# Optimization experiments

Measured on AMD Instinct MI355X. Metric: run time of the kernel, lower is better.

## Reference

```python
import jax, jax.numpy as jnp
import numpy as np

B, T, P, V, D, DINO, H, L = 32, 40, 256, 4096, 256, 384, 4, 2
HD = D // H          # head dim 64
DFF = 4 * D          # 1024
EPS = 1e-5


def setup_inputs() -> dict:
    key = jax.random.key(0)
    ks = iter(jax.random.split(key, 40))
    rn = lambda shape, s=0.02: jax.random.normal(next(ks), shape, jnp.float32) * s
    return dict(
        patches=jax.random.normal(next(ks), (B, P, DINO), jnp.float32),
        tokens=jax.random.randint(next(ks), (B, T), 0, V, jnp.int32),
        tok_emb=rn((V, D)),
        pos_emb=rn((1, T, D)),
        qkv_w=rn((L, 3 * D, D)), qkv_b=jnp.zeros((L, 3 * D), jnp.float32),
        out_w=rn((L, D, D)), out_b=jnp.zeros((L, D), jnp.float32),
        ln1_s=jnp.ones((L, D), jnp.float32), ln1_b=jnp.zeros((L, D), jnp.float32),
        w1=rn((L, DFF, D)), b1=jnp.zeros((L, DFF), jnp.float32),
        w2=rn((L, D, DFF)), b2=jnp.zeros((L, D), jnp.float32),
        ln2_s=jnp.ones((L, D), jnp.float32), ln2_b=jnp.zeros((L, D), jnp.float32),
        fus_w1=rn((D, DINO + D)), fus_b1=jnp.zeros((D,), jnp.float32),
        fus_w2=rn((D, D)), fus_b2=jnp.zeros((D,), jnp.float32),
        cls_w=rn((V, D)), cls_b=jnp.zeros((V,), jnp.float32),
    )


def _ln(x, s, b):
    m = jnp.mean(x, -1, keepdims=True)
    v = jnp.var(x, -1, keepdims=True)
    return (x - m) * jax.lax.rsqrt(v + EPS) * s + b


def _token_encoder(tokens, tok_emb, pos_emb, qkv_w, qkv_b, out_w, out_b,
                   ln1_s, ln1_b, w1, b1, w2, b2, ln2_s, ln2_b):
    # Causal full-sequence pass: output at position t equals re-running the
    # unmasked encoder on tokens[:, :t+1] and taking the last position.
    x = tok_emb[tokens] + pos_emb[:, :tokens.shape[1], :]   # [B,T,D]
    causal = jnp.triu(jnp.full((T, T), -1e9, jnp.float32), 1)  # [T,T]
    for l in range(L):  # fixed small layer count
        qkv = x @ qkv_w[l].T + qkv_b[l]                     # [B,T,3D]
        q, k, v = jnp.split(qkv, 3, axis=-1)
        q = q.reshape(B, T, H, HD).transpose(0, 2, 1, 3)    # [B,H,T,hd]
        k = k.reshape(B, T, H, HD).transpose(0, 2, 1, 3)
        v = v.reshape(B, T, H, HD).transpose(0, 2, 1, 3)
        scores = jnp.einsum('bhqd,bhkd->bhqk', q, k) / np.sqrt(HD).astype(np.float32)
        attn = jax.nn.softmax(scores + causal, axis=-1)
        ctx = jnp.einsum('bhqk,bhkd->bhqd', attn, v)        # [B,H,T,hd]
        ctx = ctx.transpose(0, 2, 1, 3).reshape(B, T, D)
        x = _ln(x + ctx @ out_w[l].T + out_b[l], ln1_s[l], ln1_b[l])
        h = jax.nn.relu(x @ w1[l].T + b1[l]) @ w2[l].T + b2[l]
        x = _ln(x + h, ln2_s[l], ln2_b[l])
    return x  # [B,T,D]


def reference(patches, tokens, tok_emb, pos_emb, qkv_w, qkv_b, out_w, out_b,
              ln1_s, ln1_b, w1, b1, w2, b2, ln2_s, ln2_b,
              fus_w1, fus_b1, fus_w2, fus_b2, cls_w, cls_b):
    enc = _token_encoder(tokens, tok_emb, pos_emb, qkv_w, qkv_b, out_w, out_b,
                         ln1_s, ln1_b, w1, b1, w2, b2, ln2_s, ln2_b)  # [B,T,D]
    # context for step 0 is zeros; step t>0 uses encoder output at position t-1
    ctx = jnp.concatenate([jnp.zeros((B, 1, D), enc.dtype), enc[:, :-1]], axis=1)  # [B,T,D]
    # fusion MLP: split the concat-linear into a patch part and a context part
    wp, wc = fus_w1[:, :DINO], fus_w1[:, DINO:]
    pproj = patches @ wp.T                                  # [B,P,D]
    cproj = ctx @ wc.T + fus_b1                             # [B,T,D]
    h = jax.nn.gelu(pproj[:, None, :, :] + cproj[:, :, None, :], approximate=False)  # [B,T,P,D]
    fused = h @ fus_w2.T + fus_b2                           # [B,T,P,D]
    # sigmoid+gather of the 4096-way logits == gather classifier rows, dot, sigmoid
    w_sel = cls_w[tokens]                                   # [B,T,D]
    b_sel = cls_b[tokens]                                   # [B,T]
    logits = jnp.einsum('btpd,btd->btp', fused, w_sel) + b_sel[:, :, None]
    probs = jax.nn.sigmoid(logits)                          # [B,T,P]
    return probs.transpose(0, 2, 1)                         # [B,P,T] == [B,256,40]
```

## Files before the change

### kernel.cpp

```cpp
#include <hip/hip_runtime.h>
#include <hip/hip_bf16.h>

#define B_ 32
#define T_ 40
#define P_ 256
#define V_ 4096
#define D_ 256
#define DINO_ 384
#define H_ 4
#define L_ 2
#define HD_ 64
#define DFF_ 1024
#define EPS_ 1e-5f

typedef __bf16 bf16;
typedef __bf16 bf16x8 __attribute__((ext_vector_type(8)));
typedef float f32x4 __attribute__((ext_vector_type(4)));

#define OFF_QKV 0
#define OFF_OUTW 393216
#define OFF_W1 524288
#define OFF_W2 1048576
#define OFF_FUS 1572864
#define WB_TOTAL 1736704
#define CONV_BLOCKS 848
#define PAT_BLOCKS 1536

__device__ __forceinline__ bf16x8 cvt8(const float* p) {
  float4 f0 = *(const float4*)p;
  float4 f1 = *(const float4*)(p + 4);
  bf16x8 v;
  v[0] = (bf16)f0.x; v[1] = (bf16)f0.y; v[2] = (bf16)f0.z; v[3] = (bf16)f0.w;
  v[4] = (bf16)f1.x; v[5] = (bf16)f1.y; v[6] = (bf16)f1.z; v[7] = (bf16)f1.w;
  return v;
}

__global__ __launch_bounds__(256) void prep_k(
    const int* __restrict__ tokens, const float* __restrict__ tok_emb,
    const float* __restrict__ pos_emb, float* __restrict__ x,
    const float* __restrict__ fus_w2, bf16* __restrict__ w2Tb,
    const float* __restrict__ qkv_w, const float* __restrict__ out_w,
    const float* __restrict__ w1, const float* __restrict__ w2,
    const float* __restrict__ fus_w1, bf16* __restrict__ wb,
    const float* __restrict__ patches, bf16* __restrict__ patb) {
  __shared__ float tile[32][33];
  int bi = blockIdx.x;
  int tid = threadIdx.x;
  if (bi < B_ * T_) {
    int t = bi % T_;
    x[bi * D_ + tid] = tok_emb[tokens[bi] * D_ + tid] + pos_emb[t * D_ + tid];
  } else if (bi < B_ * T_ + 64) {
    int tt = bi - B_ * T_;
    int bx = (tt & 7) * 32, by = (tt >> 3) * 32;
    int tx = tid & 31, ty = tid >> 5;
#pragma unroll
    for (int i = 0; i < 32; i += 8) tile[ty + i][tx] = fus_w2[(by + ty + i) * D_ + bx + tx];
    __syncthreads();
#pragma unroll
    for (int i = 0; i < 32; i += 8)
      w2Tb[(bx + ty + i) * D_ + by + tx] = (bf16)tile[tx][ty + i];
  } else if (bi < B_ * T_ + 64 + CONV_BLOCKS) {
    long f = (long)(bi - B_ * T_ - 64) * 2048 + tid * 8;
    const float* src;
    long off;
    if (f < OFF_OUTW)      { src = qkv_w;  off = f - OFF_QKV; }
    else if (f < OFF_W1)   { src = out_w;  off = f - OFF_OUTW; }
    else if (f < OFF_W2)   { src = w1;     off = f - OFF_W1; }
    else if (f < OFF_FUS)  { src = w2;     off = f - OFF_W2; }
    else                   { src = fus_w1; off = f - OFF_FUS; }
    *(bf16x8*)&wb[f] = cvt8(src + off);
  } else {
    long f = (long)(bi - B_ * T_ - 64 - CONV_BLOCKS) * 2048 + tid * 8;
    *(bf16x8*)&patb[f] = cvt8(patches + f);
  }
}

template <int ABF16, int OBF16, int RELU>
__global__ __launch_bounds__(256) void gemm64_k(
    const void* __restrict__ Av, const bf16* __restrict__ W,
    const float* __restrict__ bias, void* __restrict__ outv,
    int K, int lda, int ldw, int ldc) {
  __shared__ bf16 As[64 * 72];
  __shared__ bf16 Ws[64 * 72];
  const int tid = threadIdx.x;
  const int lane = tid & 63;
  const int wv = tid >> 6;
  const int col = lane & 15, quad = lane >> 4;
  const int bn = blockIdx.x * 64, bm = blockIdx.y * 64;
  const float* Af = (const float*)Av;
  const bf16* Ab = (const bf16*)Av;

  f32x4 acc[4];
#pragma unroll
  for (int i = 0; i < 4; ++i) acc[i] = (f32x4){0.f, 0.f, 0.f, 0.f};

  for (int kk = 0; kk < K; kk += 64) {
#pragma unroll
    for (int it = 0; it < 2; ++it) {
      int c = tid + it * 256;
      int row = c >> 3, kc = (c & 7) * 8;
      if (ABF16)
        *(bf16x8*)&As[row * 72 + kc] = *(const bf16x8*)(Ab + (long)(bm + row) * lda + kk + kc);
      else
        *(bf16x8*)&As[row * 72 + kc] = cvt8(Af + (long)(bm + row) * lda + kk + kc);
      *(bf16x8*)&Ws[row * 72 + kc] = *(const bf16x8*)(W + (long)(bn + row) * ldw + kk + kc);
    }
    __syncthreads();
#pragma unroll
    for (int ki = 0; ki < 2; ++ki) {
      bf16x8 bfr = *(const bf16x8*)&Ws[(wv * 16 + col) * 72 + ki * 32 + quad * 8];
#pragma unroll
      for (int i = 0; i < 4; ++i) {
        bf16x8 afr = *(const bf16x8*)&As[(i * 16 + col) * 72 + ki * 32 + quad * 8];
        acc[i] = __builtin_amdgcn_mfma_f32_16x16x32_bf16(afr, bfr, acc[i], 0, 0, 0);
      }
    }
    __syncthreads();
  }
  const int n = bn + wv * 16 + col;
  float bv = bias ? bias[n] : 0.0f;
#pragma unroll
  for (int i = 0; i < 4; ++i) {
#pragma unroll
    for (int r = 0; r < 4; ++r) {
      int m = bm + i * 16 + quad * 4 + r;
      float val = acc[i][r] + bv;
      if (RELU) val = fmaxf(val, 0.0f);
      if (OBF16) ((bf16*)outv)[(long)m * ldc + n] = (bf16)val;
      else ((float*)outv)[(long)m * ldc + n] = val;
    }
  }
}

template <int ABF16>
__global__ __launch_bounds__(256) void gemmln_k(
    const void* __restrict__ Av, const bf16* __restrict__ W,
    const float* __restrict__ bias, const float* __restrict__ resid,
    const float* __restrict__ lng, const float* __restrict__ lnb,
    float* __restrict__ xout, int K) {
  __shared__ bf16 As[32 * 72];
  __shared__ bf16 Ws[256 * 72];
  __shared__ float2 wred[4][32];
  const int tid = threadIdx.x;
  const int lane = tid & 63;
  const int wv = tid >> 6;
  const int col = lane & 15, quad = lane >> 4;
  const int bm = blockIdx.x * 32;
  const int srow = tid >> 3, kc = (tid & 7) * 8;
  const float* Af = (const float*)Av;
  const bf16* Ab = (const bf16*)Av;

  f32x4 acc[2][4];
#pragma unroll
  for (int mt = 0; mt < 2; ++mt)
#pragma unroll
    for (int nt = 0; nt < 4; ++nt) acc[mt][nt] = (f32x4){0.f, 0.f, 0.f, 0.f};

  for (int kk = 0; kk < K; kk += 64) {
    if (ABF16)
      *(bf16x8*)&As[srow * 72 + kc] = *(const bf16x8*)(Ab + (long)(bm + srow) * K + kk + kc);
    else
      *(bf16x8*)&As[srow * 72 + kc] = cvt8(Af + (long)(bm + srow) * K + kk + kc);
#pragma unroll
    for (int i = 0; i < 8; ++i) {
      int c = tid + i * 256;
      int r = c >> 3, k2 = (c & 7) * 8;
      *(bf16x8*)&Ws[r * 72 + k2] = *(const bf16x8*)(W + (long)r * K + kk + k2);
    }
    __syncthreads();
#pragma unroll
    for (int ki = 0; ki < 2; ++ki) {
#pragma unroll
      for (int nt = 0; nt < 4; ++nt) {
        bf16x8 bfr = *(const bf16x8*)&Ws[(wv * 64 + nt * 16 + col) * 72 + ki * 32 + quad * 8];
#pragma unroll
        for (int mt = 0; mt < 2; ++mt) {
          bf16x8 afr = *(const bf16x8*)&As[(mt * 16 + col) * 72 + ki * 32 + quad * 8];
          acc[mt][nt] = __builtin_amdgcn_mfma_f32_16x16x32_bf16(afr, bfr, acc[mt][nt], 0, 0, 0);
        }
      }
    }
    __syncthreads();
  }

  float biasv[4], gv[4], bvv[4];
#pragma unroll
  for (int nt = 0; nt < 4; ++nt) {
    int n = wv * 64 + nt * 16 + col;
    biasv[nt] = bias[n];
    gv[nt] = lng[n];
    bvv[nt] = lnb[n];
  }
  float rsum[2][4], rss[2][4];
#pragma unroll
  for (int mt = 0; mt < 2; ++mt)
#pragma unroll
    for (int r = 0; r < 4; ++r) {
      int m = bm + mt * 16 + quad * 4 + r;
      float s = 0.f, q = 0.f;
#pragma unroll
      for (int nt = 0; nt < 4; ++nt) {
        int n = wv * 64 + nt * 16 + col;
        float v = acc[mt][nt][r] + biasv[nt] + resid[(long)m * D_ + n];
        acc[mt][nt][r] = v;
        s += v;
        q += v * v;
      }
      rsum[mt][r] = s;
      rss[mt][r] = q;
    }
#pragma unroll
  for (int mk = 1; mk < 16; mk <<= 1)
#pragma unroll
    for (int mt = 0; mt < 2; ++mt)
#pragma unroll
      for (int r = 0; r < 4; ++r) {
        rsum[mt][r] += __shfl_xor(rsum[mt][r], mk);
        rss[mt][r] += __shfl_xor(rss[mt][r], mk);
      }
  if (col == 0) {
#pragma unroll
    for (int mt = 0; mt < 2; ++mt)
#pragma unroll
      for (int r = 0; r < 4; ++r) {
        float2 p; p.x = rsum[mt][r]; p.y = rss[mt][r];
        wred[wv][mt * 16 + quad * 4 + r] = p;
      }
  }
  __syncthreads();
#pragma unroll
  for (int mt = 0; mt < 2; ++mt)
#pragma unroll
    for (int r = 0; r < 4; ++r) {
      int ml = mt * 16 + quad * 4 + r;
      float s = 0.f, q = 0.f;
#pragma unroll
      for (int w = 0; w < 4; ++w) {
        float2 p = wred[w][ml];
        s += p.x;
        q += p.y;
      }
      float mean = s * (1.0f / D_);
      float inv = rsqrtf(q * (1.0f / D_) - mean * mean + EPS_);
#pragma unroll
      for (int nt = 0; nt < 4; ++nt) {
        int n = wv * 64 + nt * 16 + col;
        xout[(long)(bm + ml) * D_ + n] =
            (acc[mt][nt][r] - mean) * inv * gv[nt] + bvv[nt];
      }
    }
}

__global__ __launch_bounds__(256) void attn_k(const float* __restrict__ qkv,
                                              float* __restrict__ ctx) {
  __shared__ float q[20][HD_ + 1];
  __shared__ float k[T_][HD_ + 1];
  __shared__ float v[T_][HD_ + 1];
  __shared__ float s[20][T_ + 1];
  int h = blockIdx.x, b = blockIdx.y, zq = blockIdx.z;
  int r0 = zq * 20;
  int tid = threadIdx.x;
  for (int idx = tid; idx < T_ * HD_; idx += 256) {
    int t = idx >> 6, d = idx & 63;
    long base = (long)(b * T_ + t) * (3 * D_) + h * HD_ + d;
    k[t][d] = qkv[base + D_];
    v[t][d] = qkv[base + 2 * D_];
    if (t < 20) q[t][d] = qkv[(long)(b * T_ + r0 + t) * (3 * D_) + h * HD_ + d];
  }
  __syncthreads();
  for (int idx = tid; idx < 20 * T_; idx += 256) {
    int i = idx / T_, j = idx - i * T_;
    if (j <= r0 + i) {
      float acc = 0.f;
#pragma unroll
      for (int d = 0; d < HD_; ++d) acc += q[i][d] * k[j][d];
      s[i][j] = acc * 0.125f;
    }
  }
  __syncthreads();
  if (tid < 20) {
    int i = tid, hi = r0 + i;
    float mx = -1e30f;
    for (int j = 0; j <= hi; ++j) mx = fmaxf(mx, s[i][j]);
    float sum = 0.f;
    for (int j = 0; j <= hi; ++j) {
      float e = __expf(s[i][j] - mx);
      s[i][j] = e;
      sum += e;
    }
    float inv = 1.0f / sum;
    for (int j = 0; j <= hi; ++j) s[i][j] *= inv;
  }
  __syncthreads();
  for (int idx = tid; idx < 20 * HD_; idx += 256) {
    int i = idx >> 6, d = idx & 63;
    int hi = r0 + i;
    float acc = 0.f;
    for (int j = 0; j <= hi; ++j) acc += s[i][j] * v[j][d];
    ctx[(long)(b * T_ + hi) * D_ + h * HD_ + d] = acc;
  }
}

__global__ __launch_bounds__(256) void fuse3_k(
    const bf16* __restrict__ patb, const float* __restrict__ xbuf,
    const float* __restrict__ cls_w, const bf16* __restrict__ fusb,
    const bf16* __restrict__ w2Tb, const float* __restrict__ fus_b1,
    const int* __restrict__ tokens, float* __restrict__ pprojT,
    float* __restrict__ cw) {
  __shared__ bf16 As[64 * 72];
  __shared__ bf16 Ws[64 * 72];
  const int tid = threadIdx.x;
  const int lane = tid & 63;
  const int wv = tid >> 6;
  const int col = lane & 15, quad = lane >> 4;
  const int bn = blockIdx.x * 64;
  const int y = blockIdx.y;
  int job, bm;
  if (y < 128) { job = 0; bm = y * 64; }
  else if (y < 148) { job = 1; bm = (y - 128) * 64; }
  else { job = 2; bm = (y - 148) * 64; }
  const int K = (job == 0) ? DINO_ : D_;

  f32x4 acc[4];
#pragma unroll
  for (int i = 0; i < 4; ++i) acc[i] = (f32x4){0.f, 0.f, 0.f, 0.f};
  bf16x8 z8 = {};

  for (int kk = 0; kk < K; kk += 64) {
#pragma unroll
    for (int it = 0; it < 2; ++it) {
      int c = tid + it * 256;
      int row = c >> 3, kc = (c & 7) * 8;
      int gm = bm + row;
      bf16x8 av;
      const bf16* wp;
      if (job == 0) {
        av = *(const bf16x8*)(patb + (long)gm * DINO_ + kk + kc);
        wp = fusb + (long)(bn + row) * 640 + kk + kc;
      } else if (job == 1) {
        int t = gm % T_;
        av = (t == 0) ? z8 : cvt8(xbuf + (long)(gm - 1) * D_ + kk + kc);
        wp = fusb + 384 + (long)(bn + row) * 640 + kk + kc;
      } else {
        av = cvt8(cls_w + (long)tokens[gm] * D_ + kk + kc);
        wp = w2Tb + (long)(bn + row) * D_ + kk + kc;
      }
      *(bf16x8*)&As[row * 72 + kc] = av;
      *(bf16x8*)&Ws[row * 72 + kc] = *(const bf16x8*)wp;
    }
    __syncthreads();
#pragma unroll
    for (int ki = 0; ki < 2; ++ki) {
      bf16x8 bfr = *(const bf16x8*)&Ws[(wv * 16 + col) * 72 + ki * 32 + quad * 8];
#pragma unroll
      for (int i = 0; i < 4; ++i) {
        bf16x8 afr = *(const bf16x8*)&As[(i * 16 + col) * 72 + ki * 32 + quad * 8];
        acc[i] = __builtin_amdgcn_mfma_f32_16x16x32_bf16(afr, bfr, acc[i], 0, 0, 0);
      }
    }
    __syncthreads();
  }
  const int n = bn + wv * 16 + col;
  if (job == 0) {
#pragma unroll
    for (int i = 0; i < 4; ++i)
#pragma unroll
      for (int r = 0; r < 4; ++r) {
        int m = bm + i * 16 + quad * 4 + r;
        int b = m >> 8, p = m & 255;
        pprojT[(long)b * (D_ * P_) + (long)n * P_ + p] = acc[i][r];
      }
  } else if (job == 1) {
    float bv = fus_b1[n];
#pragma unroll
    for (int i = 0; i < 4; ++i)
#pragma unroll
      for (int r = 0; r < 4; ++r) {
        int m = bm + i * 16 + quad * 4 + r;
        cw[(long)m * (2 * D_) + n * 2] = acc[i][r] + bv;
      }
  } else {
#pragma unroll
    for (int i = 0; i < 4; ++i)
#pragma unroll
      for (int r = 0; r < 4; ++r) {
        int m = bm + i * 16 + quad * 4 + r;
        cw[(long)m * (2 * D_) + n * 2 + 1] = acc[i][r];
      }
  }
}

__global__ __launch_bounds__(256) void final_k(const float* __restrict__ pprojT,
                                               const float* __restrict__ cw,
                                               const int* __restrict__ tokens,
                                               const float* __restrict__ cls_w,
                                               const float* __restrict__ cls_b,
                                               const float* __restrict__ fus_b2,
                                               float* __restrict__ out) {
  __shared__ float2 cws[4][D_];
  int tid = threadIdx.x;
  int lane = tid & 63, wv = tid >> 6;
  int p = blockIdx.x * 64 + lane;
  int t = blockIdx.y * 4 + wv;
  int b = blockIdx.z;
  int mbase = b * T_ + blockIdx.y * 4;
  for (int idx = tid; idx < 4 * D_; idx += 256) {
    int tt = idx >> 8, e = idx & 255;
    cws[tt][e] = ((const float2*)cw)[(long)(mbase + tt) * D_ + e];
  }
  __syncthreads();

  int m = b * T_ + t;
  int tok = tokens[m];
  const float* cr = cls_w + (long)tok * D_;
  float bacc = 0.f;
#pragma unroll
  for (int i = 0; i < 4; ++i) bacc += cr[lane + i * 64] * fus_b2[lane + i * 64];
#pragma unroll
  for (int mk = 1; mk < 64; mk <<= 1) bacc += __shfl_xor(bacc, mk);
  float beff = bacc + cls_b[tok];

  const float* ppb = pprojT + (long)b * (D_ * P_);
  float acc = 0.f;
#pragma unroll 8
  for (int e = 0; e < D_; ++e) {
    float pp = ppb[e * P_ + p];
    float2 c = cws[wv][e];
    float x = pp + c.x;
    float x2 = x * x;
    float u = x * fmaf(-0.1029432f, x2, -2.3022083f);
    float ex = __builtin_amdgcn_exp2f(u);
    float r = __builtin_amdgcn_rcpf(1.0f + ex);
    acc = fmaf(x * r, c.y, acc);
  }
  float logit = acc + beff;
  float es = __builtin_amdgcn_exp2f(-1.4426950408889634f * logit);
  out[(long)(b * P_ + p) * T_ + t] = __builtin_amdgcn_rcpf(1.0f + es);
}

extern "C" void kernel_launch(void* const* d_in, const int* in_sizes, int n_in, void* d_out,
                              int out_size, void* d_ws, size_t ws_size, hipStream_t stream) {
  const float* patches = (const float*)d_in[0];
  const int* tokens = (const int*)d_in[1];
  const float* tok_emb = (const float*)d_in[2];
  const float* pos_emb = (const float*)d_in[3];
  const float* qkv_w = (const float*)d_in[4];
  const float* qkv_b = (const float*)d_in[5];
  const float* out_w = (const float*)d_in[6];
  const float* out_b = (const float*)d_in[7];
  const float* ln1_s = (const float*)d_in[8];
  const float* ln1_b = (const float*)d_in[9];
  const float* w1 = (const float*)d_in[10];
  const float* b1 = (const float*)d_in[11];
  const float* w2 = (const float*)d_in[12];
  const float* b2 = (const float*)d_in[13];
  const float* ln2_s = (const float*)d_in[14];
  const float* ln2_b = (const float*)d_in[15];
  const float* fus_w1 = (const float*)d_in[16];
  const float* fus_b1 = (const float*)d_in[17];
  const float* fus_w2 = (const float*)d_in[18];
  const float* fus_b2 = (const float*)d_in[19];
  const float* cls_w = (const float*)d_in[20];
  const float* cls_b = (const float*)d_in[21];
  float* out = (float*)d_out;

  const int MT = B_ * T_;
  float* x = (float*)d_ws;
  float* qkvbuf = x + MT * D_;
  float* attbuf = qkvbuf + MT * 3 * D_;
  float* pprojT = attbuf + MT * D_;
  float* cwbuf = pprojT + (long)B_ * D_ * P_;
  bf16* wb = (bf16*)(cwbuf + MT * D_ * 2);
  bf16* w2Tb = wb + WB_TOTAL;
  bf16* patb = w2Tb + D_ * D_;
  bf16* hb = patb + (long)B_ * P_ * DINO_;

  prep_k<<<MT + 64 + CONV_BLOCKS + PAT_BLOCKS, 256, 0, stream>>>(
      tokens, tok_emb, pos_emb, x, fus_w2, w2Tb, qkv_w, out_w, w1, w2, fus_w1, wb,
      patches, patb);

  for (int l = 0; l < L_; ++l) {
    gemm64_k<0, 0, 0><<<dim3(12, 20), 256, 0, stream>>>(
        x, wb + OFF_QKV + (long)l * 3 * D_ * D_, qkv_b + l * 3 * D_, qkvbuf,
        D_, D_, D_, 3 * D_);
    attn_k<<<dim3(H_, B_, 2), 256, 0, stream>>>(qkvbuf, attbuf);
    gemmln_k<0><<<40, 256, 0, stream>>>(
        attbuf, wb + OFF_OUTW + (long)l * D_ * D_, out_b + l * D_, x,
        ln1_s + l * D_, ln1_b + l * D_, x, D_);
    gemm64_k<0, 1, 1><<<dim3(16, 20), 256, 0, stream>>>(
        x, wb + OFF_W1 + (long)l * DFF_ * D_, b1 + l * DFF_, hb, D_, D_, D_, DFF_);
    gemmln_k<1><<<40, 256, 0, stream>>>(
        hb, wb + OFF_W2 + (long)l * D_ * DFF_, b2 + l * D_, x,
        ln2_s + l * D_, ln2_b + l * D_, x, DFF_);
  }

  fuse3_k<<<dim3(4, 168), 256, 0, stream>>>(patb, x, cls_w, wb + OFF_FUS, w2Tb,
                                            fus_b1, tokens, pprojT, cwbuf);

  final_k<<<dim3(4, 10, 32), 256, 0, stream>>>(pprojT, cwbuf, tokens, cls_w, cls_b,
                                               fus_b2, out);
}
```

Before: 284.9 us.

## Split fused GEMM+LayerNorm into small-tile GEMM plus separate LayerNorm kernel

New measurement: 270.2 us. -5.2%, faster.

```diff
diff --git a/kernel.cpp b/kernel.cpp
--- a/kernel.cpp
+++ b/kernel.cpp
@@ -132,123 +132,75 @@
   }
 }
 
-template <int ABF16>
-__global__ __launch_bounds__(256) void gemmln_k(
+template <int ABF16, int RESID>
+__global__ __launch_bounds__(256) void gemm_k(
     const void* __restrict__ Av, const bf16* __restrict__ W,
     const float* __restrict__ bias, const float* __restrict__ resid,
-    const float* __restrict__ lng, const float* __restrict__ lnb,
-    float* __restrict__ xout, int K) {
+    float* __restrict__ outv, int K, int lda, int ldw, int ldc) {
   __shared__ bf16 As[32 * 72];
-  __shared__ bf16 Ws[256 * 72];
-  __shared__ float2 wred[4][32];
+  __shared__ bf16 Ws[32 * 72];
   const int tid = threadIdx.x;
   const int lane = tid & 63;
   const int wv = tid >> 6;
+  const int mi = wv & 1, ni = wv >> 1;
   const int col = lane & 15, quad = lane >> 4;
-  const int bm = blockIdx.x * 32;
+  const int bn = blockIdx.x * 32, bm = blockIdx.y * 32;
   const int srow = tid >> 3, kc = (tid & 7) * 8;
   const float* Af = (const float*)Av;
   const bf16* Ab = (const bf16*)Av;
-
-  f32x4 acc[2][4];
-#pragma unroll
-  for (int mt = 0; mt < 2; ++mt)
-#pragma unroll
-    for (int nt = 0; nt < 4; ++nt) acc[mt][nt] = (f32x4){0.f, 0.f, 0.f, 0.f};
-
+  const bf16* Wp = W + (long)(bn + srow) * ldw + kc;
+
+  f32x4 acc = {0.f, 0.f, 0.f, 0.f};
   for (int kk = 0; kk < K; kk += 64) {
     if (ABF16)
-      *(bf16x8*)&As[srow * 72 + kc] = *(const bf16x8*)(Ab + (long)(bm + srow) * K + kk + kc);
+      *(bf16x8*)&As[srow * 72 + kc] = *(const bf16x8*)(Ab + (long)(bm + srow) * lda + kk + kc);
     else
-      *(bf16x8*)&As[srow * 72 + kc] = cvt8(Af + (long)(bm + srow) * K + kk + kc);
-#pragma unroll
-    for (int i = 0; i < 8; ++i) {
-      int c = tid + i * 256;
-      int r = c >> 3, k2 = (c & 7) * 8;
-      *(bf16x8*)&Ws[r * 72 + k2] = *(const bf16x8*)(W + (long)r * K + kk + k2);
-    }
+      *(bf16x8*)&As[srow * 72 + kc] = cvt8(Af + (long)(bm + srow) * lda + kk + kc);
+    *(bf16x8*)&Ws[srow * 72 + kc] = *(const bf16x8*)(Wp + kk);
     __syncthreads();
 #pragma unroll
     for (int ki = 0; ki < 2; ++ki) {
-#pragma unroll
-      for (int nt = 0; nt < 4; ++nt) {
-        bf16x8 bfr = *(const bf16x8*)&Ws[(wv * 64 + nt * 16 + col) * 72 + ki * 32 + quad * 8];
-#pragma unroll
-        for (int mt = 0; mt < 2; ++mt) {
-          bf16x8 afr = *(const bf16x8*)&As[(mt * 16 + col) * 72 + ki * 32 + quad * 8];
-          acc[mt][nt] = __builtin_amdgcn_mfma_f32_16x16x32_bf16(afr, bfr, acc[mt][nt], 0, 0, 0);
-        }
-      }
-    }
-    __syncthreads();
-  }
-
-  float biasv[4], gv[4], bvv[4];
-#pragma unroll
-  for (int nt = 0; nt < 4; ++nt) {
-    int n = wv * 64 + nt * 16 + col;
-    biasv[nt] = bias[n];
-    gv[nt] = lng[n];
-    bvv[nt] = lnb[n];
-  }
-  float rsum[2][4], rss[2][4];
-#pragma unroll
-  for (int mt = 0; mt < 2; ++mt)
-#pragma unroll
-    for (int r = 0; r < 4; ++r) {
-      int m = bm + mt * 16 + quad * 4 + r;
-      float s = 0.f, q = 0.f;
-#pragma unroll
-      for (int nt = 0; nt < 4; ++nt) {
-        int n = wv * 64 + nt * 16 + col;
-        float v = acc[mt][nt][r] + biasv[nt] + resid[(long)m * D_ + n];
-        acc[mt][nt][r] = v;
-        s += v;
-        q += v * v;
-      }
-      rsum[mt][r] = s;
-      rss[mt][r] = q;
-    }
-#pragma unroll
-  for (int mk = 1; mk < 16; mk <<= 1)
-#pragma unroll
-    for (int mt = 0; mt < 2; ++mt)
-#pragma unroll
-      for (int r = 0; r < 4; ++r) {
-        rsum[mt][r] += __shfl_xor(rsum[mt][r], mk);
-        rss[mt][r] += __shfl_xor(rss[mt][r], mk);
-      }
-  if (col == 0) {
-#pragma unroll
-    for (int mt = 0; mt < 2; ++mt)
-#pragma unroll
-      for (int r = 0; r < 4; ++r) {
-        float2 p; p.x = rsum[mt][r]; p.y = rss[mt][r];
-        wred[wv][mt * 16 + quad * 4 + r] = p;
-      }
-  }
-  __syncthreads();
-#pragma unroll
-  for (int mt = 0; mt < 2; ++mt)
-#pragma unroll
-    for (int r = 0; r < 4; ++r) {
-      int ml = mt * 16 + quad * 4 + r;
-      float s = 0.f, q = 0.f;
-#pragma unroll
-      for (int w = 0; w < 4; ++w) {
-        float2 p = wred[w][ml];
-        s += p.x;
-        q += p.y;
-      }
-      float mean = s * (1.0f / D_);
-      float inv = rsqrtf(q * (1.0f / D_) - mean * mean + EPS_);
-#pragma unroll
-      for (int nt = 0; nt < 4; ++nt) {
-        int n = wv * 64 + nt * 16 + col;
-        xout[(long)(bm + ml) * D_ + n] =
-            (acc[mt][nt][r] - mean) * inv * gv[nt] + bvv[nt];
-      }
-    }
+      bf16x8 afr = *(const bf16x8*)&As[(mi * 16 + col) * 72 + ki * 32 + quad * 8];
+      bf16x8 bfr = *(const bf16x8*)&Ws[(ni * 16 + col) * 72 + ki * 32 + quad * 8];
+      acc = __builtin_amdgcn_mfma_f32_16x16x32_bf16(afr, bfr, acc, 0, 0, 0);
+    }
+    __syncthreads();
+  }
+  const int n = bn + ni * 16 + col;
+  float bv = bias ? bias[n] : 0.0f;
+#pragma unroll
+  for (int r = 0; r < 4; ++r) {
+    int m = bm + mi * 16 + quad * 4 + r;
+    float val = acc[r] + bv;
+    if (RESID) val += resid[(long)m * D_ + n];
+    outv[(long)m * ldc + n] = val;
+  }
+}
+
+__global__ __launch_bounds__(256) void ln_k(const float* __restrict__ s,
+                                            float* __restrict__ xout,
+                                            const float* __restrict__ g,
+                                            const float* __restrict__ be) {
+  int wv = threadIdx.x >> 6, lane = threadIdx.x & 63;
+  int m = blockIdx.x * 4 + wv;
+  float4 v = *(const float4*)(s + (long)m * D_ + lane * 4);
+  float sum = v.x + v.y + v.z + v.w;
+  float ss = v.x * v.x + v.y * v.y + v.z * v.z + v.w * v.w;
+#pragma unroll
+  for (int mk = 1; mk < 64; mk <<= 1) {
+    sum += __shfl_xor(sum, mk);
+    ss += __shfl_xor(ss, mk);
+  }
+  float mean = sum * (1.0f / D_);
+  float inv = rsqrtf(ss * (1.0f / D_) - mean * mean + EPS_);
+  float4 g4 = *(const float4*)(g + lane * 4);
+  float4 b4 = *(const float4*)(be + lane * 4);
+  float4 o;
+  o.x = (v.x - mean) * inv * g4.x + b4.x;
+  o.y = (v.y - mean) * inv * g4.y + b4.y;
+  o.z = (v.z - mean) * inv * g4.z + b4.z;
+  o.w = (v.w - mean) * inv * g4.w + b4.w;
+  *(float4*)(xout + (long)m * D_ + lane * 4) = o;
 }
 
 __global__ __launch_bounds__(256) void attn_k(const float* __restrict__ qkv,
@@ -468,7 +420,8 @@
   float* x = (float*)d_ws;
   float* qkvbuf = x + MT * D_;
   float* attbuf = qkvbuf + MT * 3 * D_;
-  float* pprojT = attbuf + MT * D_;
+  float* s = attbuf + MT * D_;
+  float* pprojT = s + MT * D_;
   float* cwbuf = pprojT + (long)B_ * D_ * P_;
   bf16* wb = (bf16*)(cwbuf + MT * D_ * 2);
   bf16* w2Tb = wb + WB_TOTAL;
@@ -484,14 +437,14 @@
         x, wb + OFF_QKV + (long)l * 3 * D_ * D_, qkv_b + l * 3 * D_, qkvbuf,
         D_, D_, D_, 3 * D_);
     attn_k<<<dim3(H_, B_, 2), 256, 0, stream>>>(qkvbuf, attbuf);
-    gemmln_k<0><<<40, 256, 0, stream>>>(
-        attbuf, wb + OFF_OUTW + (long)l * D_ * D_, out_b + l * D_, x,
-        ln1_s + l * D_, ln1_b + l * D_, x, D_);
+    gemm_k<0, 1><<<dim3(8, 40), 256, 0, stream>>>(
+        attbuf, wb + OFF_OUTW + (long)l * D_ * D_, out_b + l * D_, x, s, D_, D_, D_, D_);
+    ln_k<<<MT / 4, 256, 0, stream>>>(s, x, ln1_s + l * D_, ln1_b + l * D_);
     gemm64_k<0, 1, 1><<<dim3(16, 20), 256, 0, stream>>>(
         x, wb + OFF_W1 + (long)l * DFF_ * D_, b1 + l * DFF_, hb, D_, D_, D_, DFF_);
-    gemmln_k<1><<<40, 256, 0, stream>>>(
-        hb, wb + OFF_W2 + (long)l * D_ * DFF_, b2 + l * D_, x,
-        ln2_s + l * D_, ln2_b + l * D_, x, DFF_);
+    gemm_k<1, 1><<<dim3(8, 40), 256, 0, stream>>>(
+        hb, wb + OFF_W2 + (long)l * D_ * DFF_, b2 + l * D_, x, s, DFF_, DFF_, DFF_, D_);
+    ln_k<<<MT / 4, 256, 0, stream>>>(s, x, ln2_s + l * D_, ln2_b + l * D_);
   }
 
   fuse3_k<<<dim3(4, 168), 256, 0, stream>>>(patb, x, cls_w, wb + OFF_FUS, w2Tb,
```
